# Optimization experiments

Hardware: AMD Instinct MI355X
Metric: run time of the kernel (lower is better)

## Reference

```python
import jax, jax.numpy as jnp
import numpy as np

B, S, H = 2, 2048, 2048
NUM_HEADS, NUM_KV_HEADS, HEAD_DIM = 8, 1, 256
ROPE_THETA = 10000.0
NEG_INF = -1e9


def _rope_tables(seq_len, head_dim, base=ROPE_THETA):
    # cos/sin of shape [seq_len, head_dim], matching GemmaRotaryEmbedding
    inv_freq = 1.0 / (base ** (jnp.arange(0, head_dim, 2, dtype=jnp.float32) / head_dim))
    pos = jnp.arange(seq_len, dtype=jnp.float32)
    freqs = pos[:, None] * inv_freq[None, :]          # [S, D/2]
    emb = jnp.concatenate([freqs, freqs], axis=-1)    # [S, D]
    return jnp.cos(emb), jnp.sin(emb)


def _rotate_half(x):
    d = x.shape[-1] // 2
    return jnp.concatenate([-x[..., d:], x[..., :d]], axis=-1)


def setup_inputs() -> dict:
    key = jax.random.key(0)
    ks = jax.random.split(key, 5)
    hidden_states = jax.random.normal(ks[0], (B, S, H), dtype=jnp.float32)
    # additive causal mask: 0 where allowed, -inf above diagonal
    causal = jnp.tril(jnp.ones((S, S), dtype=bool))
    attention_mask = jnp.where(causal, 0.0, NEG_INF).astype(jnp.float32)[None, None]  # [1,1,S,S]
    sc = 1.0 / np.sqrt(H)
    Wq = jax.random.normal(ks[1], (H, NUM_HEADS * HEAD_DIM), dtype=jnp.float32) * sc
    Wk = jax.random.normal(ks[2], (H, NUM_KV_HEADS * HEAD_DIM), dtype=jnp.float32) * sc
    Wv = jax.random.normal(ks[3], (H, NUM_KV_HEADS * HEAD_DIM), dtype=jnp.float32) * sc
    Wo = jax.random.normal(ks[4], (NUM_HEADS * HEAD_DIM, H), dtype=jnp.float32) * sc
    return {"hidden_states": hidden_states, "attention_mask": attention_mask,
            "Wq": Wq, "Wk": Wk, "Wv": Wv, "Wo": Wo}


def reference(hidden_states, attention_mask, Wq, Wk, Wv, Wo):
    b, s, _ = hidden_states.shape
    g = NUM_HEADS // NUM_KV_HEADS  # query heads per kv head

    q = (hidden_states @ Wq).reshape(b, s, NUM_HEADS, HEAD_DIM).transpose(0, 2, 1, 3)      # [b,h,s,d]
    k = (hidden_states @ Wk).reshape(b, s, NUM_KV_HEADS, HEAD_DIM).transpose(0, 2, 1, 3)   # [b,kh,s,d]
    v = (hidden_states @ Wv).reshape(b, s, NUM_KV_HEADS, HEAD_DIM).transpose(0, 2, 1, 3)   # [b,kh,s,d]

    cos, sin = _rope_tables(s, HEAD_DIM)  # [s,d]
    cos = cos[None, None]                 # [1,1,s,d]
    sin = sin[None, None]
    q = q * cos + _rotate_half(q) * sin
    k = k * cos + _rotate_half(k) * sin

    # GQA attention without materializing repeated K/V: group query heads per kv head
    qg = q.reshape(b, NUM_KV_HEADS, g, s, HEAD_DIM)                       # [b,kh,g,s,d]
    scale = 1.0 / np.sqrt(HEAD_DIM)
    scores = jnp.einsum('bkgsd,bktd->bkgst', qg, k) * scale               # [b,kh,g,s,t]
    scores = scores + attention_mask[:, :, None]                          # broadcast [1,1,1,s,t]
    probs = jax.nn.softmax(scores, axis=-1)
    out = jnp.einsum('bkgst,bktd->bkgsd', probs, v)                       # [b,kh,g,s,d]
    out = out.reshape(b, NUM_HEADS, s, HEAD_DIM).transpose(0, 2, 1, 3).reshape(b, s, NUM_HEADS * HEAD_DIM)
    return out @ Wo
```

## Files before the change

### kernel.cpp

```cpp
#include <hip/hip_runtime.h>
#include <hip/hip_bf16.h>

typedef unsigned short u16;
typedef short short8 __attribute__((ext_vector_type(8)));
typedef float f32x4 __attribute__((ext_vector_type(4)));
typedef float f32x16 __attribute__((ext_vector_type(16)));
typedef u16 u16x4 __attribute__((ext_vector_type(4)));

__device__ __forceinline__ u16 f2bf(float f) {
    unsigned int u = __float_as_uint(f);
    u += 0x7fffu + ((u >> 16) & 1u);
    return (u16)(u >> 16);
}
__device__ __forceinline__ float bf2f(u16 s) {
    return __uint_as_float(((unsigned int)s) << 16);
}
__device__ __forceinline__ unsigned pack2(float lo, float hi) {
    union { __hip_bfloat162 h; unsigned u; } cv;
    cv.h = __float22bfloat162_rn(make_float2(lo, hi));
    return cv.u;
}
__device__ __forceinline__ f32x4 mfma16(short8 a, short8 b, f32x4 c) {
    return __builtin_amdgcn_mfma_f32_16x16x32_bf16(a, b, c, 0, 0, 0);
}
__device__ __forceinline__ f32x16 mfma32(short8 a, short8 b, f32x16 c) {
    return __builtin_amdgcn_mfma_f32_32x32x16_bf16(a, b, c, 0, 0, 0);
}
__device__ __forceinline__ void gld16(const void* g, void* l) {
    __builtin_amdgcn_global_load_lds(
        (const __attribute__((address_space(1))) unsigned int*)g,
        (__attribute__((address_space(3))) unsigned int*)l, 16, 0, 0);
}

#define BATCH 2
#define SEQ   2048
#define HID   2048
#define NH    8
#define HD    256
#define MROWS (BATCH * SEQ)

__global__ void k_cvt(const float* __restrict__ src, u16* __restrict__ dst, int n) {
    int i = (blockIdx.x * 256 + threadIdx.x) * 4;
    if (i >= n) return;
    float4 v = *(const float4*)(src + i);
    u16x4 o; o.x = f2bf(v.x); o.y = f2bf(v.y); o.z = f2bf(v.z); o.w = f2bf(v.w);
    *(u16x4*)(dst + i) = o;
}

__global__ __launch_bounds__(256) void k_wt(const float* __restrict__ W,
                                            u16* __restrict__ Wt, int N) {
    __shared__ float tile[64][65];
    const int k0 = blockIdx.y << 6, n0 = blockIdx.x << 6;
    const int tr = threadIdx.x >> 6, tc = threadIdx.x & 63;
#pragma unroll
    for (int i = 0; i < 16; i++)
        tile[i * 4 + tr][tc] = W[(size_t)(k0 + i * 4 + tr) * N + n0 + tc];
    __syncthreads();
#pragma unroll
    for (int i = 0; i < 16; i++) {
        int r = i * 4 + tr;
        Wt[(size_t)(n0 + r) * 2048 + k0 + tc] = f2bf(tile[tc][r]);
    }
}

__global__ __launch_bounds__(256) void k_vt(const u16* __restrict__ KVb, char* __restrict__ VS) {
    __shared__ u16 sT[64][72];
    const int bid = blockIdx.x;
    const int b = bid >> 7, kvt = (bid >> 2) & 31, dc = bid & 3;
    const int tr = threadIdx.x >> 6, tc = threadIdx.x & 63;
#pragma unroll
    for (int i = 0; i < 16; i++) {
        int kv = i * 4 + tr;
        sT[kv][tc] = KVb[((size_t)(b * SEQ + kvt * 64 + kv) << 9) + 256 + (dc << 6) + tc];
    }
    __syncthreads();
    char* obase = VS + ((size_t)b << 20) + (size_t)kvt * 32768;
#pragma unroll
    for (int e = 0; e < 2; e++) {
        int u = threadIdx.x * 2 + e;
        int dl = u >> 3, kvc = u & 7;
        union { u16 h[8]; uint4 q; } pk;
#pragma unroll
        for (int j = 0; j < 8; j++) pk.h[j] = sT[kvc * 8 + j][dl];
        int byte = dl * 512 + ((((dc << 7) + (kvc << 4))) ^ ((dl & 31) << 4));
        *(uint4*)(obase + byte) = pk.q;
    }
}

template<int FUSEQKV>
__global__ __launch_bounds__(256) void k_gemm(const u16* __restrict__ A,
                                              const u16* __restrict__ Bt,
                                              u16* __restrict__ Cq,
                                              u16* __restrict__ Ckv,
                                              float* __restrict__ Cf,
                                              int K, int nbx) {
    const int cpx = gridDim.x >> 3;
    const int t8  = (blockIdx.x & 7) * cpx + (blockIdx.x >> 3);
    const int m0 = (t8 / nbx) << 7;
    const int n0 = (t8 % nbx) << 7;

    const int tid = threadIdx.x, lane = tid & 63, wave = tid >> 6;
    const int g = lane >> 4, c = lane & 15;
    const int wrow = (wave >> 1) << 6, wcol = (wave & 1) << 6;

    __shared__ __align__(16) u16 sA[2][128 * 64];
    __shared__ __align__(16) u16 sB[2][128 * 64];

    const int srow = lane >> 3;
    const int scol = ((lane & 7) ^ srow) << 3;
    const u16* gA = A  + (size_t)(m0 + wave * 32 + srow) * K + scol;
    const u16* gB = Bt + (size_t)(n0 + wave * 32 + srow) * K + scol;
    const int lofs = wave * 32 * 64;

    f32x4 acc[4][4] = {};
    const int nt = K >> 6;

#define STAGE(t, bi)                                                         \
    {                                                                        \
        const int k0s = (t) << 6;                                            \
        _Pragma("unroll")                                                    \
        for (int i = 0; i < 4; i++) {                                        \
            gld16(gA + k0s + (size_t)i * 8 * K, sA[bi] + lofs + i * 8 * 64); \
            gld16(gB + k0s + (size_t)i * 8 * K, sB[bi] + lofs + i * 8 * 64); \
        }                                                                    \
    }

    STAGE(0, 0);
    for (int t = 0; t < nt; t++) {
        const int bi = t & 1;
        __syncthreads();
        if (t + 1 < nt) STAGE(t + 1, bi ^ 1);
#pragma unroll
        for (int ks = 0; ks < 2; ks++) {
            short8 aF[4], bF[4];
#pragma unroll
            for (int tt = 0; tt < 4; tt++) {
                const int ar = wrow + tt * 16 + c;
                const int br = wcol + tt * 16 + c;
                const int coff = ks * 64 + g * 16;
                aF[tt] = *(const short8*)((const char*)sA[bi] + ar * 128 + (coff ^ ((ar & 7) << 4)));
                bF[tt] = *(const short8*)((const char*)sB[bi] + br * 128 + (coff ^ ((br & 7) << 4)));
            }
#pragma unroll
            for (int mt = 0; mt < 4; mt++)
#pragma unroll
                for (int ntc = 0; ntc < 4; ntc++)
                    acc[mt][ntc] = mfma16(aF[mt], bF[ntc], acc[mt][ntc]);
        }
    }
#undef STAGE

#pragma unroll
    for (int mt = 0; mt < 4; mt++)
#pragma unroll
        for (int ntc = 0; ntc < 4; ntc++)
#pragma unroll
            for (int r = 0; r < 4; r++) {
                int row = m0 + wrow + mt * 16 + g * 4 + r;
                int col = n0 + wcol + ntc * 16 + c;
                float v = acc[mt][ntc][r];
                if (FUSEQKV) {
                    if (col < 2048) Cq [(size_t)row * 2048 + col] = f2bf(v);
                    else            Ckv[(size_t)row * 512 + (col - 2048)] = f2bf(v);
                } else {
                    Cf[(size_t)row * 2048 + col] = v;
                }
            }
}

__global__ void k_rope(u16* __restrict__ Qb, const u16* __restrict__ KVb,
                       char* __restrict__ KS) {
    int idx = blockIdx.x * 256 + threadIdx.x;
    const int QP = MROWS * NH * 128;
    if (idx < QP) {
        int row  = idx >> 10;
        int rest = idx & 1023;
        int h = rest >> 7, d = rest & 127;
        u16* base = Qb + (size_t)row * HID + h * HD + d;
        int pos = row & (SEQ - 1);
        float invf = __expf(-(float)d * (9.2103403719761836f / 128.0f));
        float ang = (float)pos * invf;
        float sn, cs; __sincosf(ang, &sn, &cs);
        float x0 = bf2f(base[0]);
        float x1 = bf2f(base[128]);
        base[0]   = f2bf(x0 * cs - x1 * sn);
        base[128] = f2bf(x1 * cs + x0 * sn);
    } else {
        int j = idx - QP;
        int row = j >> 7, d = j & 127;
        const u16* src = KVb + (size_t)row * 512 + d;
        int pos = row & (SEQ - 1);
        float invf = __expf(-(float)d * (9.2103403719761836f / 128.0f));
        float ang = (float)pos * invf;
        float sn, cs; __sincosf(ang, &sn, &cs);
        float x0 = bf2f(src[0]);
        float x1 = bf2f(src[128]);
        int bb = row >> 11, sr = row & 2047;
        char* obase = KS + ((size_t)bb << 20) + (size_t)(sr >> 6) * 32768 + (sr & 63) * 512;
        int xr = ((sr & 31) << 4);
        *(u16*)(obase + (((d << 1))        ^ xr)) = f2bf(x0 * cs - x1 * sn);
        *(u16*)(obase + (((d << 1) + 256)  ^ xr)) = f2bf(x1 * cs + x0 * sn);
    }
}

__global__ __launch_bounds__(256, 2) void k_attn(const u16* __restrict__ Q,
                                                 const char* __restrict__ KS,
                                                 const char* __restrict__ VS,
                                                 u16* __restrict__ Oa) {
    const int tid  = threadIdx.x;
    const int lane = tid & 63;
    const int wave = tid >> 6;
    const int l31  = lane & 31;
    const int hv   = lane >> 5;

    const int bid   = blockIdx.x;
    const int bh    = bid & 15;
    const int qpair = (bid >> 4) & 15;
    const int qidx  = (bid >> 8) ? (31 - qpair) : qpair;
    const int qb    = qidx << 6;
    const int b = bh >> 3, head = bh & 7;

    __shared__ __align__(16) char smem[66560];
    char*  const pK  = smem;
    char*  const pV  = smem + 32768;
    float* const sML = (float*)(smem + 65536);

    const int qg = qb + ((wave >> 1) << 5) + l31;
    short8 qf[16];
    {
        const u16* qptr = Q + (size_t)(b * SEQ + qg) * HID + head * HD + (hv << 3);
#pragma unroll
        for (int ks = 0; ks < 16; ks++)
            qf[ks] = *(const short8*)(qptr + (ks << 4));
    }

    f32x16 o[8] = {};
    float m = -1e30f, l = 0.f;

    const char* kgb = KS + ((size_t)b << 20);
    const char* vgb = VS + ((size_t)b << 20);
    const int   kxor  = l31 << 4;
    const char* kbase = pK + (((wave & 1) << 5) + l31) * 512;

    const int nt = qidx + 1;
    for (int t = 0; t < nt; t++) {
        __syncthreads();
#pragma unroll
        for (int i = 0; i < 8; i++) {
            int chunk = (i << 2) + wave;
            gld16(kgb + (size_t)t * 32768 + chunk * 1024 + lane * 16, pK + chunk * 1024);
            gld16(vgb + (size_t)t * 32768 + chunk * 1024 + lane * 16, pV + chunk * 1024);
        }
        __syncthreads();

        f32x16 sv0 = {}, sv1 = {};
#pragma unroll
        for (int ks = 0; ks < 16; ks += 2) {
            short8 kf0 = *(const short8*)(kbase + (((ks << 5) + (hv << 4)) ^ kxor));
            short8 kf1 = *(const short8*)(kbase + ((((ks + 1) << 5) + (hv << 4)) ^ kxor));
            sv0 = mfma32(kf0, qf[ks], sv0);
            sv1 = mfma32(kf1, qf[ks + 1], sv1);
        }
        f32x16 s = sv0 + sv1;

        float v[16];
        float mx = -3.0e38f;
        const bool diag = (t == nt - 1);
#pragma unroll
        for (int r = 0; r < 16; r++) {
            float x = s[r] * 0.0625f;
            if (diag) {
                int kvg = (t << 6) + ((wave & 1) << 5) + (r & 3) + ((r >> 2) << 3) + (hv << 2);
                if (kvg > qg) x = -3.0e38f;
            }
            v[r] = x;
            mx = fmaxf(mx, x);
        }
        mx = fmaxf(mx, __shfl_xor(mx, 32));
        if (!__all(mx <= m + 8.0f)) {
            float mn = fmaxf(m, mx);
            float sc = __expf(m - mn);
            l *= sc;
#pragma unroll
            for (int r = 0; r < 16; r++) {
                float scr = __shfl(sc, (r & 3) + ((r >> 2) << 3) + (hv << 2));
#pragma unroll
                for (int dt = 0; dt < 8; dt++) o[dt][r] *= scr;
            }
            m = mn;
        }
        float rs = 0.f;
#pragma unroll
        for (int r = 0; r < 16; r++) { v[r] = __expf(v[r] - m); rs += v[r]; }
        rs += __shfl_xor(rs, 32);
        l += rs;

        unsigned wd[8], pw[8];
#pragma unroll
        for (int i = 0; i < 8; i++) wd[i] = pack2(v[2 * i], v[2 * i + 1]);
#pragma unroll
        for (int i = 0; i < 8; i++) pw[i] = (unsigned)__shfl_xor((int)wd[i], 32);

#pragma unroll
        for (int ks2 = 0; ks2 < 2; ks2++) {
            union { unsigned u[4]; short8 s8; } fr;
            const int o4 = ks2 << 2;
            fr.u[0] = hv ? pw[o4 + 2] : wd[o4 + 0];
            fr.u[1] = hv ? pw[o4 + 3] : wd[o4 + 1];
            fr.u[2] = hv ? wd[o4 + 2] : pw[o4 + 0];
            fr.u[3] = hv ? wd[o4 + 3] : pw[o4 + 1];
            const int vcol = ((wave & 1) << 6) + (ks2 << 5) + (hv << 4);
#pragma unroll
            for (int dt = 0; dt < 8; dt++) {
                int row  = ((dt & 1) << 5) + l31;
                int colb = ((dt >> 1) << 7) + vcol;
                short8 vf = *(const short8*)(pV + row * 512 + (colb ^ kxor));
                o[dt] = mfma32(fr.s8, vf, o[dt]);
            }
        }
    }

    __syncthreads();
    if (lane < 32) {
        sML[(wave << 6) + (l31 << 1)]     = m;
        sML[(wave << 6) + (l31 << 1) + 1] = l;
    }
    __syncthreads();
    float m1 = sML[((wave ^ 1) << 6) + (l31 << 1)];
    float l1 = sML[((wave ^ 1) << 6) + (l31 << 1) + 1];
    float M  = fmaxf(m, m1);
    float e0 = __expf(m - M), e1 = __expf(m1 - M);
    float fac = e0 / (l * e0 + l1 * e1);
    float facr[16];
#pragma unroll
    for (int r = 0; r < 16; r++)
        facr[r] = __shfl(fac, (r & 3) + ((r >> 2) << 3) + (hv << 2));
#pragma unroll
    for (int dt = 0; dt < 8; dt++)
#pragma unroll
        for (int r = 0; r < 16; r++) o[dt][r] *= facr[r];

    float* sO = (float*)smem;
    if (wave & 1) {
#pragma unroll
        for (int dt = 0; dt < 8; dt++)
#pragma unroll
            for (int r = 0; r < 16; r++) {
                int q = (r & 3) + ((r >> 2) << 3) + (hv << 2);
                sO[((wave >> 1) << 13) + (q << 8) + (dt << 5) + l31] = o[dt][r];
            }
    }
    __syncthreads();
    if (!(wave & 1)) {
#pragma unroll
        for (int dt = 0; dt < 8; dt++)
#pragma unroll
            for (int r = 0; r < 16; r++) {
                int q = (r & 3) + ((r >> 2) << 3) + (hv << 2);
                float val = o[dt][r] + sO[((wave >> 1) << 13) + (q << 8) + (dt << 5) + l31];
                Oa[(size_t)(b * SEQ + qb + ((wave >> 1) << 5) + q) * HID
                   + head * HD + (dt << 5) + l31] = f2bf(val);
            }
    }
}

extern "C" void kernel_launch(void* const* d_in, const int* in_sizes, int n_in,
                              void* d_out, int out_size, void* d_ws, size_t ws_size,
                              hipStream_t stream) {
    const float* hidden = (const float*)d_in[0];
    const float* Wq = (const float*)d_in[2];
    const float* Wk = (const float*)d_in[3];
    const float* Wv = (const float*)d_in[4];
    const float* Wo = (const float*)d_in[5];
    float* out = (float*)d_out;

    char* ws = (char*)d_ws;
    u16* hid_bf = (u16*)(ws);
    u16* Wqkvt  = (u16*)(ws + (16u << 20));
    u16* Wot    = (u16*)(ws + (26u << 20));
    u16* Qb     = (u16*)(ws + (34u << 20));
    u16* KVb    = (u16*)(ws + (50u << 20));
    u16* Ab     = (u16*)(ws + (54u << 20));
    char* KS    = ws;
    char* VS    = ws + (2u << 20);

    k_cvt<<<8192, 256, 0, stream>>>(hidden, hid_bf, MROWS * HID);
    k_wt <<<dim3(32, 32), 256, 0, stream>>>(Wq, Wqkvt, 2048);
    k_wt <<<dim3(4, 32),  256, 0, stream>>>(Wk, Wqkvt + (size_t)2048 * 2048, 256);
    k_wt <<<dim3(4, 32),  256, 0, stream>>>(Wv, Wqkvt + (size_t)2304 * 2048, 256);
    k_wt <<<dim3(32, 32), 256, 0, stream>>>(Wo, Wot, 2048);

    k_gemm<1><<<640, 256, 0, stream>>>(hid_bf, Wqkvt, Qb, KVb, nullptr, 2048, 20);

    k_rope<<<18432, 256, 0, stream>>>(Qb, KVb, KS);
    k_vt  <<<256, 256, 0, stream>>>(KVb, VS);

    k_attn<<<512, 256, 0, stream>>>(Qb, KS, VS, Ab);

    k_gemm<0><<<512, 256, 0, stream>>>(Ab, Wot, nullptr, nullptr, out, 2048, 16);
}
```

Baseline: 240.7 us.

## Split KV range for long causal query tiles and merge partial outputs

New measurement: 255.4 us. 6.1% more time.

```diff
diff --git a/kernel.cpp b/kernel.cpp
--- a/kernel.cpp
+++ b/kernel.cpp
@@ -38,6 +38,7 @@
 #define NH    8
 #define HD    256
 #define MROWS (BATCH * SEQ)
+#define PCH   4194304
 
 __global__ void k_cvt(const float* __restrict__ src, u16* __restrict__ dst, int n) {
     int i = (blockIdx.x * 256 + threadIdx.x) * 4;
@@ -206,19 +207,30 @@
 __global__ __launch_bounds__(256, 2) void k_attn(const u16* __restrict__ Q,
                                                  const char* __restrict__ KS,
                                                  const char* __restrict__ VS,
-                                                 u16* __restrict__ Oa) {
+                                                 u16* __restrict__ Oa,
+                                                 u16* __restrict__ Pf,
+                                                 float2* __restrict__ MLp) {
     const int tid  = threadIdx.x;
     const int lane = tid & 63;
     const int wave = tid >> 6;
     const int l31  = lane & 31;
     const int hv   = lane >> 5;
 
-    const int bid   = blockIdx.x;
-    const int bh    = bid & 15;
-    const int qpair = (bid >> 4) & 15;
-    const int qidx  = (bid >> 8) ? (31 - qpair) : qpair;
-    const int qb    = qidx << 6;
+    const int bid  = blockIdx.x;
+    const int bh   = bid & 15;
+    const int unit = bid >> 4;
     const int b = bh >> 3, head = bh & 7;
+
+    int qi, t0, tE, chunk, split;
+    if (unit < 16) { qi = unit; chunk = 0; split = 0; t0 = 0; tE = qi + 1; }
+    else {
+        int v = unit - 16;
+        qi = 16 + (v >> 1); chunk = v & 1; split = 1;
+        int half = (qi + 1) >> 1;
+        t0 = chunk ? half : 0;
+        tE = chunk ? (qi + 1) : half;
+    }
+    const int qb = qi << 6;
 
     __shared__ __align__(16) char smem[66560];
     char*  const pK  = smem;
@@ -242,14 +254,13 @@
     const int   kxor  = l31 << 4;
     const char* kbase = pK + (((wave & 1) << 5) + l31) * 512;
 
-    const int nt = qidx + 1;
-    for (int t = 0; t < nt; t++) {
+    for (int t = t0; t < tE; t++) {
         __syncthreads();
 #pragma unroll
         for (int i = 0; i < 8; i++) {
-            int chunk = (i << 2) + wave;
-            gld16(kgb + (size_t)t * 32768 + chunk * 1024 + lane * 16, pK + chunk * 1024);
-            gld16(vgb + (size_t)t * 32768 + chunk * 1024 + lane * 16, pV + chunk * 1024);
+            int ch = (i << 2) + wave;
+            gld16(kgb + (size_t)t * 32768 + ch * 1024 + lane * 16, pK + ch * 1024);
+            gld16(vgb + (size_t)t * 32768 + ch * 1024 + lane * 16, pV + ch * 1024);
         }
         __syncthreads();
 
@@ -265,7 +276,7 @@
 
         float v[16];
         float mx = -3.0e38f;
-        const bool diag = (t == nt - 1);
+        const bool diag = (t == qi);
 #pragma unroll
         for (int r = 0; r < 16; r++) {
             float x = s[r] * 0.0625f;
@@ -330,7 +341,8 @@
     float l1 = sML[((wave ^ 1) << 6) + (l31 << 1) + 1];
     float M  = fmaxf(m, m1);
     float e0 = __expf(m - M), e1 = __expf(m1 - M);
-    float fac = e0 / (l * e0 + l1 * e1);
+    float denomL = l * e0 + l1 * e1;
+    float fac = split ? e0 : (e0 / denomL);
     float facr[16];
 #pragma unroll
     for (int r = 0; r < 16; r++)
@@ -339,6 +351,11 @@
     for (int dt = 0; dt < 8; dt++)
 #pragma unroll
         for (int r = 0; r < 16; r++) o[dt][r] *= facr[r];
+
+    if (split && !(wave & 1) && lane < 32) {
+        int mlrow = (bh * 16 + (qi - 16)) * 64 + ((wave >> 1) << 5) + l31;
+        MLp[chunk * 16384 + mlrow] = make_float2(M, denomL);
+    }
 
     float* sO = (float*)smem;
     if (wave & 1) {
@@ -358,10 +375,38 @@
             for (int r = 0; r < 16; r++) {
                 int q = (r & 3) + ((r >> 2) << 3) + (hv << 2);
                 float val = o[dt][r] + sO[((wave >> 1) << 13) + (q << 8) + (dt << 5) + l31];
-                Oa[(size_t)(b * SEQ + qb + ((wave >> 1) << 5) + q) * HID
-                   + head * HD + (dt << 5) + l31] = f2bf(val);
-            }
-    }
+                int qrow = ((wave >> 1) << 5) + q;
+                if (split) {
+                    size_t prow = (size_t)((bh * 16 + (qi - 16)) * 64 + qrow);
+                    Pf[(size_t)chunk * PCH + prow * 256 + (dt << 5) + l31] = f2bf(val);
+                } else {
+                    Oa[(size_t)(b * SEQ + qb + qrow) * HID
+                       + head * HD + (dt << 5) + l31] = f2bf(val);
+                }
+            }
+    }
+}
+
+__global__ __launch_bounds__(256) void k_mg(const u16* __restrict__ Pf,
+                                            const float2* __restrict__ MLp,
+                                            u16* __restrict__ Oa) {
+    int gid = blockIdx.x * 256 + threadIdx.x;
+    int rowp = gid >> 6;
+    int d4 = (gid & 63) << 2;
+    float2 A = MLp[rowp], B = MLp[16384 + rowp];
+    float Mf = fmaxf(A.x, B.x);
+    float ea = __expf(A.x - Mf), eb = __expf(B.x - Mf);
+    float inv = 1.0f / (A.y * ea + B.y * eb);
+    u16x4 pa = *(const u16x4*)(Pf + (size_t)rowp * 256 + d4);
+    u16x4 pb = *(const u16x4*)(Pf + (size_t)PCH + (size_t)rowp * 256 + d4);
+    u16x4 ov;
+#pragma unroll
+    for (int j = 0; j < 4; j++)
+        ov[j] = f2bf((bf2f(pa[j]) * ea + bf2f(pb[j]) * eb) * inv);
+    int bh = rowp >> 10, qim = (rowp >> 6) & 15, r = rowp & 63;
+    int b = bh >> 3, head = bh & 7;
+    size_t orow = (size_t)(b * SEQ + (16 + qim) * 64 + r) * HID + head * HD + d4;
+    *(u16x4*)(Oa + orow) = ov;
 }
 
 extern "C" void kernel_launch(void* const* d_in, const int* in_sizes, int n_in,
@@ -383,6 +428,8 @@
     u16* Ab     = (u16*)(ws + (54u << 20));
     char* KS    = ws;
     char* VS    = ws + (2u << 20);
+    u16* Pf     = (u16*)(ws + (4u << 20));
+    float2* MLp = (float2*)(ws + (50u << 20));
 
     k_cvt<<<8192, 256, 0, stream>>>(hidden, hid_bf, MROWS * HID);
     k_wt <<<dim3(32, 32), 256, 0, stream>>>(Wq, Wqkvt, 2048);
@@ -395,7 +442,8 @@
     k_rope<<<18432, 256, 0, stream>>>(Qb, KVb, KS);
     k_vt  <<<256, 256, 0, stream>>>(KVb, VS);
 
-    k_attn<<<512, 256, 0, stream>>>(Qb, KS, VS, Ab);
+    k_attn<<<768, 256, 0, stream>>>(Qb, KS, VS, Ab, Pf, MLp);
+    k_mg  <<<4096, 256, 0, stream>>>(Pf, MLp, Ab);
 
     k_gemm<0><<<512, 256, 0, stream>>>(Ab, Wot, nullptr, nullptr, out, 2048, 16);
 }
```
